# Performance work log

Hardware: AMD Instinct MI355X
Metric: run time of the kernel (lower is better)

## Reference

```python
import jax, jax.numpy as jnp
import numpy as np

N = 100000      # num nodes
C = 64          # in_channels
E = 1600000     # num edges
H = 8           # heads
L = 3           # num_layers -> L-1 per-layer params
NEG_SLOPE = 0.01  # F.leaky_relu default


def setup_inputs() -> dict:
    key = jax.random.key(0)
    ks = jax.random.split(key, 8)
    x = jax.random.normal(ks[0], (N, C), dtype=jnp.float32)
    edge_index = jax.random.randint(ks[1], (2, E), 0, N, dtype=jnp.int64)
    structural_features = jax.random.normal(ks[2], (E, 4), dtype=jnp.float32)
    # psi modeled as a frozen Linear(4 -> 2C)
    psi_w = jax.random.normal(ks[3], (2 * C, 4), dtype=jnp.float32) * 0.1
    psi_b = jax.random.normal(ks[4], (2 * C,), dtype=jnp.float32) * 0.1
    delta_w = jax.random.normal(ks[5], (L - 1, 2 * C), dtype=jnp.float32) * 0.01
    u = jax.random.normal(ks[6], (L - 1, 2 * C), dtype=jnp.float32)
    gamma_h = jnp.ones((L - 1, H), dtype=jnp.float32)
    return {"x": x, "edge_index": edge_index,
            "structural_features": structural_features, "layer_idx": 1,
            "psi_w": psi_w, "psi_b": psi_b,
            "delta_w": delta_w, "u": u, "gamma_h": gamma_h}


def reference(x, edge_index, structural_features, layer_idx,
              psi_w, psi_b, delta_w, u, gamma_h):
    # psi runs under torch.no_grad -> stop_gradient
    w0 = jax.lax.stop_gradient(structural_features @ psi_w.T + psi_b)   # [E, 2C]
    coef = w0 + delta_w[layer_idx] + u[layer_idx]                        # [E, 2C]
    row, col = edge_index[0], edge_index[1]
    # (cat([x[row], x[col]], -1) * coef).sum(-1), without materializing the concat
    s = jnp.sum(x[row] * coef[:, :C], axis=-1) \
        + jnp.sum(x[col] * coef[:, C:], axis=-1)                         # [E]
    base_pred = jax.nn.leaky_relu(s, NEG_SLOPE)                          # [E]
    y_hat_h = gamma_h[layer_idx][None, :] * base_pred[:, None]           # [E, H]
    return y_hat_h
```

## Files before the change

kernel.cpp:

```cpp
#include <hip/hip_runtime.h>
#include <hip/hip_fp16.h>

#define N_NODES 100000
#define CCH 64
#define E_EDGES 1600000
#define HH 8
#define ETHR 1024

typedef float v4f __attribute__((ext_vector_type(4)));

union RecU {
    uint4  v;
    __half h[8];
};

__global__ __launch_bounds__(256) void node_pre(
    const float* __restrict__ x,
    const int* __restrict__ layer_idx_p,
    const float* __restrict__ psi_w,
    const float* __restrict__ psi_b,
    const float* __restrict__ delta_w,
    const float* __restrict__ u,
    uint4* __restrict__ recs)
{
    __shared__ float4 s_w0[CCH];
    __shared__ float4 s_w1[CCH];
    __shared__ float  s_b0[CCH];
    __shared__ float  s_b1[CCH];

    int li = layer_idx_p[0];
    for (int i = threadIdx.x; i < 2 * CCH; i += blockDim.x) {
        float4 w = make_float4(psi_w[i * 4 + 0], psi_w[i * 4 + 1],
                               psi_w[i * 4 + 2], psi_w[i * 4 + 3]);
        float bb = psi_b[i] + delta_w[li * 2 * CCH + i] + u[li * 2 * CCH + i];
        if (i < CCH) { s_w0[i] = w; s_b0[i] = bb; }
        else         { s_w1[i - CCH] = w; s_b1[i - CCH] = bb; }
    }
    __syncthreads();

    int n = blockIdx.x * blockDim.x + threadIdx.x;
    if (n >= N_NODES) return;

    const float4* xr = (const float4*)(x + (size_t)n * CCH);
    float a0 = 0, a1 = 0, a2 = 0, a3 = 0, aq = 0;
    float c0 = 0, c1 = 0, c2 = 0, c3 = 0, cq = 0;
#pragma unroll
    for (int it = 0; it < CCH / 4; ++it) {
        float4 xv4 = xr[it];
        float xv[4] = { xv4.x, xv4.y, xv4.z, xv4.w };
#pragma unroll
        for (int j = 0; j < 4; ++j) {
            int c = it * 4 + j;
            float xv_ = xv[j];
            float4 w0 = s_w0[c];
            float4 w1 = s_w1[c];
            a0 += xv_ * w0.x; a1 += xv_ * w0.y; a2 += xv_ * w0.z; a3 += xv_ * w0.w;
            aq += xv_ * s_b0[c];
            c0 += xv_ * w1.x; c1 += xv_ * w1.y; c2 += xv_ * w1.z; c3 += xv_ * w1.w;
            cq += xv_ * s_b1[c];
        }
    }
    RecU rs;
    rs.h[0] = __float2half_rn(a0); rs.h[1] = __float2half_rn(a1);
    rs.h[2] = __float2half_rn(a2); rs.h[3] = __float2half_rn(a3);
    rs.h[4] = __float2half_rn(aq);
    rs.h[5] = __half(0.0f); rs.h[6] = __half(0.0f); rs.h[7] = __half(0.0f);
    RecU rd;
    rd.h[0] = __float2half_rn(c0); rd.h[1] = __float2half_rn(c1);
    rd.h[2] = __float2half_rn(c2); rd.h[3] = __float2half_rn(c3);
    rd.h[4] = __float2half_rn(cq);
    rd.h[5] = __half(0.0f); rd.h[6] = __half(0.0f); rd.h[7] = __half(0.0f);
    recs[2 * (size_t)n]     = rs.v;
    recs[2 * (size_t)n + 1] = rd.v;
}

__global__ __launch_bounds__(ETHR) void edge_k(
    const int* __restrict__ ei,
    const float* __restrict__ sf,
    const int* __restrict__ layer_idx_p,
    const float* __restrict__ gamma_h,
    const uint4* __restrict__ recs,
    float* __restrict__ out)
{
    __shared__ float s_g[HH];
    __shared__ float s_b[ETHR];

    if (threadIdx.x < HH) {
        int li = layer_idx_p[0];
        s_g[threadIdx.x] = gamma_h[li * HH + threadIdx.x];
    }

    int e  = blockIdx.x * ETHR + threadIdx.x;
    int ee = (e < E_EDGES) ? e : (E_EDGES - 1);

    int row = __builtin_nontemporal_load(ei + ee);
    int col = __builtin_nontemporal_load(ei + E_EDGES + ee);
    v4f f   = __builtin_nontemporal_load((const v4f*)sf + ee);

    RecU rs; rs.v = recs[2 * (size_t)row];
    RecU rd; rd.v = recs[2 * (size_t)col + 1];

    float s = f.x * (__half2float(rs.h[0]) + __half2float(rd.h[0]))
            + f.y * (__half2float(rs.h[1]) + __half2float(rd.h[1]))
            + f.z * (__half2float(rs.h[2]) + __half2float(rd.h[2]))
            + f.w * (__half2float(rs.h[3]) + __half2float(rd.h[3]))
            + __half2float(rs.h[4]) + __half2float(rd.h[4]);
    float base = (s > 0.0f) ? s : 0.01f * s;

    s_b[threadIdx.x] = base;
    __syncthreads();

    int t = threadIdx.x;
    float b0v = s_b[t >> 1];
    float b1v = s_b[(t >> 1) + (ETHR / 2)];
    const int go = (t & 1) * 4;
    float g0 = s_g[go + 0], g1 = s_g[go + 1], g2 = s_g[go + 2], g3 = s_g[go + 3];
    v4f o0 = { g0 * b0v, g1 * b0v, g2 * b0v, g3 * b0v };
    v4f o1 = { g0 * b1v, g1 * b1v, g2 * b1v, g3 * b1v };

    size_t vbase = (size_t)blockIdx.x * (2 * ETHR);
    v4f* op = (v4f*)out;
    int e0 = blockIdx.x * ETHR + (t >> 1);
    if (e0 < E_EDGES)
        __builtin_nontemporal_store(o0, op + vbase + t);
    if (e0 + ETHR / 2 < E_EDGES)
        __builtin_nontemporal_store(o1, op + vbase + ETHR + t);
}

extern "C" void kernel_launch(void* const* d_in, const int* in_sizes, int n_in,
                              void* d_out, int out_size, void* d_ws, size_t ws_size,
                              hipStream_t stream) {
    const float* x       = (const float*)d_in[0];
    const int*   ei      = (const int*)d_in[1];
    const float* sf      = (const float*)d_in[2];
    const int*   li      = (const int*)d_in[3];
    const float* psi_w   = (const float*)d_in[4];
    const float* psi_b   = (const float*)d_in[5];
    const float* delta_w = (const float*)d_in[6];
    const float* u       = (const float*)d_in[7];
    const float* gamma_h = (const float*)d_in[8];
    float* out = (float*)d_out;

    uint4* recs = (uint4*)d_ws;

    node_pre<<<(N_NODES + 255) / 256, 256, 0, stream>>>(
        x, li, psi_w, psi_b, delta_w, u, recs);

    edge_k<<<(E_EDGES + ETHR - 1) / ETHR, ETHR, 0, stream>>>(
        ei, sf, li, gamma_h, recs, out);
}
```

Measured before the change: 144.1 us.

## Stage node records in output buffer tail and compute tail edges directly

The fp16 node records now live in the last part of the output buffer instead of the separate workspace. That region is exactly the size of the outputs for the final 100000 edges. The main edge kernel covers only the first edges. A new wave-per-edge tail kernel then computes the remaining edges straight from x and psi, overwriting the record storage. This avoids using the workspace, but it adds a third launch and a tail pass that does full-precision 64-channel gathers with wave reductions, which costs more per edge than the record path.

```diff
diff --git a/kernel.cpp b/kernel.cpp
--- a/kernel.cpp
+++ b/kernel.cpp
@@ -6,6 +6,8 @@
 #define E_EDGES 1600000
 #define HH 8
 #define ETHR 1024
+#define TAIL_E 100000
+#define EMAIN (E_EDGES - TAIL_E)
 
 typedef float v4f __attribute__((ext_vector_type(4)));
 
@@ -91,7 +93,7 @@
     }
 
     int e  = blockIdx.x * ETHR + threadIdx.x;
-    int ee = (e < E_EDGES) ? e : (E_EDGES - 1);
+    int ee = (e < EMAIN) ? e : (EMAIN - 1);
 
     int row = __builtin_nontemporal_load(ei + ee);
     int col = __builtin_nontemporal_load(ei + E_EDGES + ee);
@@ -121,10 +123,55 @@
     size_t vbase = (size_t)blockIdx.x * (2 * ETHR);
     v4f* op = (v4f*)out;
     int e0 = blockIdx.x * ETHR + (t >> 1);
-    if (e0 < E_EDGES)
+    if (e0 < EMAIN)
         __builtin_nontemporal_store(o0, op + vbase + t);
-    if (e0 + ETHR / 2 < E_EDGES)
+    if (e0 + ETHR / 2 < EMAIN)
         __builtin_nontemporal_store(o1, op + vbase + ETHR + t);
+}
+
+__global__ __launch_bounds__(256) void edge_tail(
+    const float* __restrict__ x,
+    const int* __restrict__ ei,
+    const float* __restrict__ sf,
+    const int* __restrict__ layer_idx_p,
+    const float* __restrict__ psi_w,
+    const float* __restrict__ psi_b,
+    const float* __restrict__ delta_w,
+    const float* __restrict__ u,
+    const float* __restrict__ gamma_h,
+    float* __restrict__ out)
+{
+    int li   = layer_idx_p[0];
+    int lane = threadIdx.x & 63;
+    int wv   = (blockIdx.x * blockDim.x + threadIdx.x) >> 6;
+    if (wv >= TAIL_E) return;
+    int e = EMAIN + wv;
+
+    float4 w0 = *(const float4*)(psi_w + (size_t)lane * 4);
+    float4 w1 = *(const float4*)(psi_w + (size_t)(CCH + lane) * 4);
+    int ofs = li * 2 * CCH;
+    float b0 = psi_b[lane]       + delta_w[ofs + lane]       + u[ofs + lane];
+    float b1 = psi_b[CCH + lane] + delta_w[ofs + CCH + lane] + u[ofs + CCH + lane];
+
+    int row = ei[e];
+    int col = ei[E_EDGES + e];
+    float4 f4 = *(const float4*)(sf + (size_t)e * 4);
+
+    float c0 = w0.x * f4.x + w0.y * f4.y + w0.z * f4.z + w0.w * f4.w + b0;
+    float c1 = w1.x * f4.x + w1.y * f4.y + w1.z * f4.z + w1.w * f4.w + b1;
+
+    float xs = x[(size_t)row * CCH + lane];
+    float xd = x[(size_t)col * CCH + lane];
+    float part = xs * c0 + xd * c1;
+
+#pragma unroll
+    for (int off = 32; off > 0; off >>= 1)
+        part += __shfl_down(part, off);
+    float s = __shfl(part, 0);
+    float base = (s > 0.0f) ? s : 0.01f * s;
+
+    if (lane < HH)
+        out[(size_t)e * HH + lane] = gamma_h[li * HH + lane] * base;
 }
 
 extern "C" void kernel_launch(void* const* d_in, const int* in_sizes, int n_in,
@@ -141,11 +188,14 @@
     const float* gamma_h = (const float*)d_in[8];
     float* out = (float*)d_out;
 
-    uint4* recs = (uint4*)d_ws;
+    uint4* recs = (uint4*)(out + (size_t)EMAIN * HH);
 
     node_pre<<<(N_NODES + 255) / 256, 256, 0, stream>>>(
         x, li, psi_w, psi_b, delta_w, u, recs);
 
-    edge_k<<<(E_EDGES + ETHR - 1) / ETHR, ETHR, 0, stream>>>(
+    edge_k<<<(EMAIN + ETHR - 1) / ETHR, ETHR, 0, stream>>>(
         ei, sf, li, gamma_h, recs, out);
-}
+
+    edge_tail<<<(TAIL_E * 64) / 256, 256, 0, stream>>>(
+        x, ei, sf, li, psi_w, psi_b, delta_w, u, gamma_h, out);
+}
```

After: 172.9 us. 1.2x slower.
